# Kernel optimization log

Measured on AMD Instinct MI355X. Metric: run time of the kernel, lower is better.

## Reference

```python
import jax, jax.numpy as jnp
import numpy as np

N_NODES = 50000
N_RELS = 8
IN_DIM = 128
OUT_DIM = 128
N_EDGES = 800000


def setup_inputs() -> dict:
    key = jax.random.key(0)
    k1, k2, k3, k4 = jax.random.split(key, 4)
    src = jax.random.randint(k1, (N_EDGES,), 0, N_NODES, dtype=jnp.int64 if jax.config.jax_enable_x64 else jnp.int32)
    rel = jax.random.randint(k2, (N_EDGES,), 0, N_RELS, dtype=src.dtype)
    tgt = jax.random.randint(k3, (N_EDGES,), 0, N_NODES, dtype=src.dtype)
    triples = jnp.stack([src, rel, tgt], axis=1)  # (E, 3) like torch layout (s, r, t)
    features = jax.random.normal(k4, (N_NODES, IN_DIM), dtype=jnp.float32)
    weights = jax.random.normal(jax.random.fold_in(key, 1), (N_RELS, IN_DIM, OUT_DIM), dtype=jnp.float32) * (1.0 / np.sqrt(IN_DIM))
    bias = jnp.zeros((OUT_DIM,), dtype=jnp.float32)
    return {"triples": triples, "features": features, "weights": weights, "bias": bias}


def reference(triples, features, weights, bias):
    # RGCN-NC forward, horizontal stacking (featured mode):
    #   out[t] = sum_{(s,r,t) in E} (1/c_{t,r}) * features[s] @ W[r] + bias
    # where c_{t,r} = #edges sharing the same (relation, target) pair,
    # matching sum_sparse(..., row_normalisation=False) on the (n x r*n) adjacency.
    src, rel, tgt = triples[:, 0], triples[:, 1], triples[:, 2]
    n = features.shape[0]
    r = weights.shape[0]
    e = triples.shape[0]

    # per-(rel, tgt) edge counts -> 1/c normalization per edge
    key = rel * n + tgt  # column index of horizontally stacked adjacency
    counts = jax.ops.segment_sum(jnp.ones((e,), dtype=features.dtype), key, num_segments=r * n)
    vals = 1.0 / counts[key]  # (E,)

    # dense per-relation transform: H[r] = X @ W[r]   (r, n, out)
    h = jnp.einsum('ni,rio->rno', features, weights)

    # gather per-edge messages, scale, scatter-add into targets
    msgs = h[rel, src] * vals[:, None]  # (E, out)
    out = jax.ops.segment_sum(msgs, tgt, num_segments=n)  # (n, out)
    return out + bias
```

## Files before the change

kernel.cpp:

```cpp
#include <hip/hip_runtime.h>
#include <hip/hip_bf16.h>

#define N_NODES 50000
#define N_RELS 8
#define IN_DIM 128
#define OUT_DIM 128
#define N_EDGES 800000
#define NR (N_NODES * N_RELS)
#define KDIM (N_RELS * IN_DIM)
#define SCAN_ELEMS 2048
#define SCAN_NBLK ((NR + SCAN_ELEMS - 1) / SCAN_ELEMS)
#define FUSE_BLKS 1563
#define CNT_BLKS ((N_EDGES / 4 + 255) / 256)
#define CW_BLKS ((N_RELS * IN_DIM * OUT_DIM + 255) / 256)
#define FB_BLKS ((N_NODES * IN_DIM / 8 + 255) / 256)

typedef __attribute__((ext_vector_type(8))) short bf16x8;
typedef __attribute__((ext_vector_type(4))) float floatx4;
typedef __attribute__((ext_vector_type(4))) unsigned int uintx4;

__device__ inline unsigned short f2bf(float f) {
    unsigned u = __builtin_bit_cast(unsigned, f);
    u += 0x7fff + ((u >> 16) & 1);
    return (unsigned short)(u >> 16);
}
__device__ inline float bflo(unsigned u) {
    return __builtin_bit_cast(float, u << 16);
}
__device__ inline float bfhi(unsigned u) {
    return __builtin_bit_cast(float, u & 0xffff0000u);
}

__global__ void prep_kernel(const int* __restrict__ tri, const float* __restrict__ W,
                            const float* __restrict__ features,
                            int* __restrict__ cnt, unsigned short* __restrict__ Wtf,
                            unsigned short* __restrict__ featB) {
    const int b = blockIdx.x;
    if (b < CNT_BLKS) {
        int t = b * 256 + threadIdx.x;
        if (t >= N_EDGES / 4) return;
        const int4* tri4 = (const int4*)tri;
        int4 a = tri4[3 * t], v = tri4[3 * t + 1], c = tri4[3 * t + 2];
        atomicAdd(&cnt[a.z * N_RELS + a.y], 1);
        atomicAdd(&cnt[v.y * N_RELS + v.x], 1);
        atomicAdd(&cnt[c.x * N_RELS + v.w], 1);
        atomicAdd(&cnt[c.w * N_RELS + c.z], 1);
    } else if (b < CNT_BLKS + CW_BLKS) {
        int idx = (b - CNT_BLKS) * 256 + threadIdx.x;
        if (idx >= N_RELS * IN_DIM * OUT_DIM) return;
        int e  = idx & 7;
        int l  = (idx >> 3) & 63;
        int ks = (idx >> 9) & 31;
        int nt = idx >> 14;
        int o = nt * 16 + (l & 15);
        int k = ks * 32 + (l >> 4) * 8 + e;
        Wtf[idx] = f2bf(W[(k >> 7) * (IN_DIM * OUT_DIM) + (k & 127) * OUT_DIM + o]);
    } else {
        int t = (b - CNT_BLKS - CW_BLKS) * 256 + threadIdx.x;
        if (t >= N_NODES * IN_DIM / 8) return;
        const float4* f4 = (const float4*)features;
        float4 x = f4[2 * t], y = f4[2 * t + 1];
        uint4 o;
        o.x = (unsigned)f2bf(x.x) | ((unsigned)f2bf(x.y) << 16);
        o.y = (unsigned)f2bf(x.z) | ((unsigned)f2bf(x.w) << 16);
        o.z = (unsigned)f2bf(y.x) | ((unsigned)f2bf(y.y) << 16);
        o.w = (unsigned)f2bf(y.z) | ((unsigned)f2bf(y.w) << 16);
        ((uint4*)featB)[t] = o;
    }
}

__global__ void scan_part(const int* __restrict__ cnt, int* __restrict__ bsum) {
    __shared__ int s[256];
    int b = blockIdx.x, t = threadIdx.x;
    int base = b * SCAN_ELEMS + t * 8;
    int sum = 0;
#pragma unroll
    for (int k = 0; k < 8; ++k) {
        int i = base + k;
        sum += (i < NR) ? cnt[i] : 0;
    }
    s[t] = sum; __syncthreads();
    for (int off = 128; off > 0; off >>= 1) {
        if (t < off) s[t] += s[t + off];
        __syncthreads();
    }
    if (t == 0) bsum[b] = s[0];
}

__global__ __launch_bounds__(256) void scan_fused(
    const int* __restrict__ cnt, const int* __restrict__ bsum,
    int* __restrict__ segOff, int* __restrict__ cursor)
{
    __shared__ int s[256];
    __shared__ int sboff;
    const int b = blockIdx.x, t = threadIdx.x;

    int vb = (t < SCAN_NBLK) ? bsum[t] : 0;
    s[t] = vb; __syncthreads();
    for (int off = 1; off < 256; off <<= 1) {
        int x = (t >= off) ? s[t - off] : 0;
        __syncthreads();
        s[t] += x;
        __syncthreads();
    }
    if (t == 0) sboff = (b == 0) ? 0 : s[b - 1];
    __syncthreads();
    const int boff = sboff;

    const int base = b * SCAN_ELEMS + t * 8;
    int v[8]; int sum = 0;
#pragma unroll
    for (int k = 0; k < 8; ++k) {
        int i = base + k;
        v[k] = (i < NR) ? cnt[i] : 0;
        sum += v[k];
    }
    s[t] = sum; __syncthreads();
    for (int off = 1; off < 256; off <<= 1) {
        int x = (t >= off) ? s[t - off] : 0;
        __syncthreads();
        s[t] += x;
        __syncthreads();
    }
    int run = boff + s[t] - sum;
#pragma unroll
    for (int k = 0; k < 8; ++k) {
        int i = base + k;
        if (i < NR) { segOff[i] = run; cursor[i] = run; run += v[k]; }
    }
    if (b == 0 && t == 0) segOff[NR] = N_EDGES;
}

__global__ void scatter_kernel(const int* __restrict__ tri, int* __restrict__ cursor,
                               int* __restrict__ sortedSrc) {
    int t = blockIdx.x * 256 + threadIdx.x;
    if (t >= N_EDGES / 4) return;
    const int4* tri4 = (const int4*)tri;
    int4 a = tri4[3 * t], v = tri4[3 * t + 1], c = tri4[3 * t + 2];
    int p0 = atomicAdd(&cursor[a.z * N_RELS + a.y], 1);
    int p1 = atomicAdd(&cursor[v.y * N_RELS + v.x], 1);
    int p2 = atomicAdd(&cursor[c.x * N_RELS + v.w], 1);
    int p3 = atomicAdd(&cursor[c.w * N_RELS + c.z], 1);
    sortedSrc[p0] = a.x;
    sortedSrc[p1] = a.w;
    sortedSrc[p2] = v.z;
    sortedSrc[p3] = c.y;
}

__global__ __launch_bounds__(512, 8) void fused_kernel(
    const int* __restrict__ sortedSrc, const int* __restrict__ segOff,
    const unsigned short* __restrict__ featB,
    const unsigned short* __restrict__ Wtf,
    const float* __restrict__ bias,
    float* __restrict__ out)
{
    __shared__ __align__(16) unsigned short Atile[32 * 512];
    const int tid = threadIdx.x;
    const int wave = tid >> 6, lane = tid & 63;
    const int q = lane >> 4, l16 = lane & 15;
    const int m0 = blockIdx.x * 32;
    const int wm = wave & 1, wn = wave >> 1;

    floatx4 acc[2];
#pragma unroll
    for (int nt = 0; nt < 2; ++nt) acc[nt] = (floatx4){0.f, 0.f, 0.f, 0.f};

    const unsigned short* fb = featB + 8 * l16;

#pragma unroll
    for (int p = 0; p < 2; ++p) {
        for (int i = 0; i < 4; ++i) {
            const int nl = wave * 4 + i;
            const int node = m0 + nl;
            if (node < N_NODES) {
                int bnd = 0;
                if (lane < 5) bnd = segOff[node * N_RELS + 4 * p + lane];
                int sg[5];
#pragma unroll
                for (int k = 0; k < 5; ++k) sg[k] = __shfl(bnd, k);

                const int e0 = sg[0], eN = sg[4];
                int srcw = 0;
                if (e0 + lane < eN) srcw = sortedSrc[e0 + lane];

                const int s0v = sg[q], s1v = sg[q + 1];
                const int len = s1v - s0v;
                int m0x = __shfl_xor(len, 16);
                int jm = (len > m0x) ? len : m0x;
                int m1x = __shfl_xor(jm, 32);
                const int jmax = (jm > m1x) ? jm : m1x;
                float a0 = 0.f, a1 = 0.f, a2 = 0.f, a3 = 0.f;
                float a4 = 0.f, a5 = 0.f, a6 = 0.f, a7 = 0.f;
                for (int j = 0; j < jmax; j += 2) {
                    const int ea = s0v + j;
                    const int ia = ea - e0;
                    const int swina = __shfl(srcw, ia & 63);
                    const int ib = ia + 1;
                    const int swinb = __shfl(srcw, ib & 63);
                    const bool pa = j < len;
                    const bool pb = j + 1 < len;
                    int srca = 0, srcb = 0;
                    if (pa) srca = (ia < 64) ? swina : sortedSrc[ea];
                    if (pb) srcb = (ib < 64) ? swinb : sortedSrc[ea + 1];
                    uint4 ua = *(const uint4*)&fb[srca * IN_DIM];
                    uint4 ub = *(const uint4*)&fb[srcb * IN_DIM];
                    if (pa) {
                        a0 += bflo(ua.x); a1 += bfhi(ua.x);
                        a2 += bflo(ua.y); a3 += bfhi(ua.y);
                        a4 += bflo(ua.z); a5 += bfhi(ua.z);
                        a6 += bflo(ua.w); a7 += bfhi(ua.w);
                    }
                    if (pb) {
                        a0 += bflo(ub.x); a1 += bfhi(ub.x);
                        a2 += bflo(ub.y); a3 += bfhi(ub.y);
                        a4 += bflo(ub.z); a5 += bfhi(ub.z);
                        a6 += bflo(ub.w); a7 += bfhi(ub.w);
                    }
                }
                const float inv = (len > 0) ? 1.0f / (float)len : 0.0f;
                uintx4 pk;
                pk[0] = (unsigned)f2bf(a0 * inv) | ((unsigned)f2bf(a1 * inv) << 16);
                pk[1] = (unsigned)f2bf(a2 * inv) | ((unsigned)f2bf(a3 * inv) << 16);
                pk[2] = (unsigned)f2bf(a4 * inv) | ((unsigned)f2bf(a5 * inv) << 16);
                pk[3] = (unsigned)f2bf(a6 * inv) | ((unsigned)f2bf(a7 * inv) << 16);
                const int us = (q * 16 + l16) ^ (nl & 15);
                *(uintx4*)&Atile[(nl * 64 + us) * 8] = pk;
            }
        }
        __syncthreads();

        __builtin_amdgcn_s_setprio(1);
#pragma unroll
        for (int ksl = 0; ksl < 16; ++ksl) {
            const int ks = p * 16 + ksl;
            const int r = wm * 16 + l16;
            const int us = (ksl * 4 + q) ^ (r & 15);
            bf16x8 a = *(const bf16x8*)&Atile[(r * 64 + us) * 8];
#pragma unroll
            for (int nt = 0; nt < 2; ++nt) {
                const int ntg = wn * 2 + nt;
                bf16x8 b = *(const bf16x8*)&Wtf[(size_t)((ntg * 32 + ks) * 64 + lane) * 8];
                acc[nt] = __builtin_amdgcn_mfma_f32_16x16x32_bf16(a, b, acc[nt], 0, 0, 0);
            }
        }
        __builtin_amdgcn_s_setprio(0);
        __syncthreads();
    }

    float* fbuf = (float*)Atile;
#pragma unroll
    for (int nt = 0; nt < 2; ++nt) {
        const int o = (wn * 2 + nt) * 16 + l16;
        const float bv = bias[o];
#pragma unroll
        for (int j = 0; j < 4; ++j) {
            const int r = wm * 16 + q * 4 + j;
            fbuf[r * 128 + o] = acc[nt][j] + bv;
        }
    }
    __syncthreads();
    {
        const int row = tid >> 4;
        const int col = (tid & 15) * 8;
        const int node = m0 + row;
        if (node < N_NODES) {
            floatx4 w0 = *(const floatx4*)&fbuf[row * 128 + col];
            floatx4 w1 = *(const floatx4*)&fbuf[row * 128 + col + 4];
            float* po = &out[(size_t)node * OUT_DIM + col];
            __builtin_nontemporal_store(w0, (floatx4*)po);
            __builtin_nontemporal_store(w1, (floatx4*)(po + 4));
        }
    }
}

extern "C" void kernel_launch(void* const* d_in, const int* in_sizes, int n_in,
                              void* d_out, int out_size, void* d_ws, size_t ws_size,
                              hipStream_t stream)
{
    const int*   tri      = (const int*)d_in[0];
    const float* features = (const float*)d_in[1];
    const float* W        = (const float*)d_in[2];
    const float* bias     = (const float*)d_in[3];
    float* out = (float*)d_out;

    char* ws = (char*)d_ws;
    unsigned short* Wtf = (unsigned short*)ws; ws += (size_t)OUT_DIM * KDIM * 2;
    int* cnt       = (int*)ws; ws += (size_t)NR * 4;
    int* segOff    = (int*)ws; ws += (size_t)(NR + 4) * 4;
    int* cursor    = (int*)ws; ws += (size_t)NR * 4;
    int* bsum      = (int*)ws; ws += (size_t)SCAN_NBLK * 4;
    int* sortedSrc = (int*)ws; ws += (size_t)N_EDGES * 4;
    unsigned short* featB = (unsigned short*)ws; ws += (size_t)N_NODES * IN_DIM * 2;
    (void)ws_size; (void)in_sizes; (void)n_in; (void)out_size;

    hipMemsetAsync(cnt, 0, NR * sizeof(int), stream);
    prep_kernel<<<CNT_BLKS + CW_BLKS + FB_BLKS, 256, 0, stream>>>(tri, W, features, cnt, Wtf, featB);
    scan_part<<<SCAN_NBLK, 256, 0, stream>>>(cnt, bsum);
    scan_fused<<<SCAN_NBLK, 256, 0, stream>>>(cnt, bsum, segOff, cursor);
    scatter_kernel<<<CNT_BLKS, 256, 0, stream>>>(tri, cursor, sortedSrc);
    fused_kernel<<<FUSE_BLKS, 512, 0, stream>>>(sortedSrc, segOff, featB, Wtf, bias, out);
}
```

Baseline: 256.5 us.

## Merge count, scan and scatter prelude into one persistent kernel with grid barriers

Replaces the four preprocessing launches (prep, two-pass scan, scatter) with a single kernel of 782 blocks of 512 threads. The phases are separated by software grid barriers built on atomic counters. This removes several kernel launch gaps and the tail drain between dependent stages. The barrier relies on all blocks being co-resident, so a different occupancy could deadlock it, and thread 0 of each block spin-waits on a global atomic.

```diff
diff --git a/kernel.cpp b/kernel.cpp
--- a/kernel.cpp
+++ b/kernel.cpp
@@ -8,12 +8,11 @@
 #define N_EDGES 800000
 #define NR (N_NODES * N_RELS)
 #define KDIM (N_RELS * IN_DIM)
-#define SCAN_ELEMS 2048
-#define SCAN_NBLK ((NR + SCAN_ELEMS - 1) / SCAN_ELEMS)
+#define PRE_NB 782
+#define PRE_T 512
+#define PRE_THREADS (PRE_NB * PRE_T)
+#define SCB 391
 #define FUSE_BLKS 1563
-#define CNT_BLKS ((N_EDGES / 4 + 255) / 256)
-#define CW_BLKS ((N_RELS * IN_DIM * OUT_DIM + 255) / 256)
-#define FB_BLKS ((N_NODES * IN_DIM / 8 + 255) / 256)
 
 typedef __attribute__((ext_vector_type(8))) short bf16x8;
 typedef __attribute__((ext_vector_type(4))) float floatx4;
@@ -31,23 +30,34 @@
     return __builtin_bit_cast(float, u & 0xffff0000u);
 }
 
-__global__ void prep_kernel(const int* __restrict__ tri, const float* __restrict__ W,
-                            const float* __restrict__ features,
-                            int* __restrict__ cnt, unsigned short* __restrict__ Wtf,
-                            unsigned short* __restrict__ featB) {
+__device__ __forceinline__ void grid_bar(int* __restrict__ bar, int idx, int nblk) {
+    __syncthreads();
+    if (threadIdx.x == 0) {
+        __threadfence();
+        atomicAdd(&bar[idx], 1);
+        while (__hip_atomic_load(&bar[idx], __ATOMIC_RELAXED,
+                                 __HIP_MEMORY_SCOPE_AGENT) < nblk)
+            __builtin_amdgcn_s_sleep(1);
+        __threadfence();
+    }
+    __syncthreads();
+}
+
+__global__ __launch_bounds__(512, 8) void prelude_kernel(
+    const int* __restrict__ tri, const float* __restrict__ features,
+    const float* __restrict__ W,
+    unsigned short* __restrict__ Wtf, unsigned short* __restrict__ featB,
+    int* __restrict__ cnt, int* __restrict__ bar,
+    int* __restrict__ segOff, int* __restrict__ cursor,
+    int* __restrict__ bsum, int* __restrict__ sortedSrc)
+{
+    __shared__ int s_int[512];
+    const int tid = threadIdx.x;
     const int b = blockIdx.x;
-    if (b < CNT_BLKS) {
-        int t = b * 256 + threadIdx.x;
-        if (t >= N_EDGES / 4) return;
-        const int4* tri4 = (const int4*)tri;
-        int4 a = tri4[3 * t], v = tri4[3 * t + 1], c = tri4[3 * t + 2];
-        atomicAdd(&cnt[a.z * N_RELS + a.y], 1);
-        atomicAdd(&cnt[v.y * N_RELS + v.x], 1);
-        atomicAdd(&cnt[c.x * N_RELS + v.w], 1);
-        atomicAdd(&cnt[c.w * N_RELS + c.z], 1);
-    } else if (b < CNT_BLKS + CW_BLKS) {
-        int idx = (b - CNT_BLKS) * 256 + threadIdx.x;
-        if (idx >= N_RELS * IN_DIM * OUT_DIM) return;
+    const int gid = b * PRE_T + tid;
+
+    if (gid < N_RELS * IN_DIM * OUT_DIM) {
+        const int idx = gid;
         int e  = idx & 7;
         int l  = (idx >> 3) & 63;
         int ks = (idx >> 9) & 31;
@@ -55,9 +65,8 @@
         int o = nt * 16 + (l & 15);
         int k = ks * 32 + (l >> 4) * 8 + e;
         Wtf[idx] = f2bf(W[(k >> 7) * (IN_DIM * OUT_DIM) + (k & 127) * OUT_DIM + o]);
-    } else {
-        int t = (b - CNT_BLKS - CW_BLKS) * 256 + threadIdx.x;
-        if (t >= N_NODES * IN_DIM / 8) return;
+    }
+    for (int t = gid; t < N_NODES * IN_DIM / 8; t += PRE_THREADS) {
         const float4* f4 = (const float4*)features;
         float4 x = f4[2 * t], y = f4[2 * t + 1];
         uint4 o;
@@ -67,84 +76,72 @@
         o.w = (unsigned)f2bf(y.z) | ((unsigned)f2bf(y.w) << 16);
         ((uint4*)featB)[t] = o;
     }
-}
-
-__global__ void scan_part(const int* __restrict__ cnt, int* __restrict__ bsum) {
-    __shared__ int s[256];
-    int b = blockIdx.x, t = threadIdx.x;
-    int base = b * SCAN_ELEMS + t * 8;
-    int sum = 0;
-#pragma unroll
-    for (int k = 0; k < 8; ++k) {
-        int i = base + k;
-        sum += (i < NR) ? cnt[i] : 0;
-    }
-    s[t] = sum; __syncthreads();
-    for (int off = 128; off > 0; off >>= 1) {
-        if (t < off) s[t] += s[t + off];
-        __syncthreads();
-    }
-    if (t == 0) bsum[b] = s[0];
-}
-
-__global__ __launch_bounds__(256) void scan_fused(
-    const int* __restrict__ cnt, const int* __restrict__ bsum,
-    int* __restrict__ segOff, int* __restrict__ cursor)
-{
-    __shared__ int s[256];
-    __shared__ int sboff;
-    const int b = blockIdx.x, t = threadIdx.x;
-
-    int vb = (t < SCAN_NBLK) ? bsum[t] : 0;
-    s[t] = vb; __syncthreads();
-    for (int off = 1; off < 256; off <<= 1) {
-        int x = (t >= off) ? s[t - off] : 0;
-        __syncthreads();
-        s[t] += x;
-        __syncthreads();
-    }
-    if (t == 0) sboff = (b == 0) ? 0 : s[b - 1];
-    __syncthreads();
-    const int boff = sboff;
-
-    const int base = b * SCAN_ELEMS + t * 8;
-    int v[8]; int sum = 0;
-#pragma unroll
-    for (int k = 0; k < 8; ++k) {
-        int i = base + k;
-        v[k] = (i < NR) ? cnt[i] : 0;
-        sum += v[k];
-    }
-    s[t] = sum; __syncthreads();
-    for (int off = 1; off < 256; off <<= 1) {
-        int x = (t >= off) ? s[t - off] : 0;
-        __syncthreads();
-        s[t] += x;
-        __syncthreads();
-    }
-    int run = boff + s[t] - sum;
-#pragma unroll
-    for (int k = 0; k < 8; ++k) {
-        int i = base + k;
-        if (i < NR) { segOff[i] = run; cursor[i] = run; run += v[k]; }
-    }
-    if (b == 0 && t == 0) segOff[NR] = N_EDGES;
-}
-
-__global__ void scatter_kernel(const int* __restrict__ tri, int* __restrict__ cursor,
-                               int* __restrict__ sortedSrc) {
-    int t = blockIdx.x * 256 + threadIdx.x;
-    if (t >= N_EDGES / 4) return;
-    const int4* tri4 = (const int4*)tri;
-    int4 a = tri4[3 * t], v = tri4[3 * t + 1], c = tri4[3 * t + 2];
-    int p0 = atomicAdd(&cursor[a.z * N_RELS + a.y], 1);
-    int p1 = atomicAdd(&cursor[v.y * N_RELS + v.x], 1);
-    int p2 = atomicAdd(&cursor[c.x * N_RELS + v.w], 1);
-    int p3 = atomicAdd(&cursor[c.w * N_RELS + c.z], 1);
-    sortedSrc[p0] = a.x;
-    sortedSrc[p1] = a.w;
-    sortedSrc[p2] = v.z;
-    sortedSrc[p3] = c.y;
+    if (gid < N_EDGES / 4) {
+        const int4* tri4 = (const int4*)tri;
+        int4 a = tri4[3 * gid], v = tri4[3 * gid + 1], c = tri4[3 * gid + 2];
+        atomicAdd(&cnt[a.z * N_RELS + a.y], 1);
+        atomicAdd(&cnt[v.y * N_RELS + v.x], 1);
+        atomicAdd(&cnt[c.x * N_RELS + v.w], 1);
+        atomicAdd(&cnt[c.w * N_RELS + c.z], 1);
+    }
+    grid_bar(bar, 0, PRE_NB);
+
+    if (b < SCB) {
+        const int base = b * 1024 + tid * 2;
+        int v0 = (base     < NR) ? cnt[base]     : 0;
+        int v1 = (base + 1 < NR) ? cnt[base + 1] : 0;
+        s_int[tid] = v0 + v1;
+        __syncthreads();
+        for (int off = 256; off > 0; off >>= 1) {
+            if (tid < off) s_int[tid] += s_int[tid + off];
+            __syncthreads();
+        }
+        if (tid == 0) bsum[b] = s_int[0];
+    }
+    grid_bar(bar, 1, PRE_NB);
+
+    if (b < SCB) {
+        int vb = (tid < SCB) ? bsum[tid] : 0;
+        s_int[tid] = vb; __syncthreads();
+        for (int off = 1; off < 512; off <<= 1) {
+            int x = (tid >= off) ? s_int[tid - off] : 0;
+            __syncthreads();
+            s_int[tid] += x;
+            __syncthreads();
+        }
+        const int boff = (b == 0) ? 0 : s_int[b - 1];
+        __syncthreads();
+
+        const int base = b * 1024 + tid * 2;
+        int v0 = (base     < NR) ? cnt[base]     : 0;
+        int v1 = (base + 1 < NR) ? cnt[base + 1] : 0;
+        const int sum = v0 + v1;
+        s_int[tid] = sum; __syncthreads();
+        for (int off = 1; off < 512; off <<= 1) {
+            int x = (tid >= off) ? s_int[tid - off] : 0;
+            __syncthreads();
+            s_int[tid] += x;
+            __syncthreads();
+        }
+        int run = boff + s_int[tid] - sum;
+        if (base < NR)     { segOff[base] = run;     cursor[base] = run;     run += v0; }
+        if (base + 1 < NR) { segOff[base + 1] = run; cursor[base + 1] = run; }
+        if (b == 0 && tid == 0) segOff[NR] = N_EDGES;
+    }
+    grid_bar(bar, 2, PRE_NB);
+
+    if (gid < N_EDGES / 4) {
+        const int4* tri4 = (const int4*)tri;
+        int4 a = tri4[3 * gid], v = tri4[3 * gid + 1], c = tri4[3 * gid + 2];
+        int p0 = atomicAdd(&cursor[a.z * N_RELS + a.y], 1);
+        int p1 = atomicAdd(&cursor[v.y * N_RELS + v.x], 1);
+        int p2 = atomicAdd(&cursor[c.x * N_RELS + v.w], 1);
+        int p3 = atomicAdd(&cursor[c.w * N_RELS + c.z], 1);
+        sortedSrc[p0] = a.x;
+        sortedSrc[p1] = a.w;
+        sortedSrc[p2] = v.z;
+        sortedSrc[p3] = c.y;
+    }
 }
 
 __global__ __launch_bounds__(512, 8) void fused_kernel(
@@ -286,17 +283,17 @@
     char* ws = (char*)d_ws;
     unsigned short* Wtf = (unsigned short*)ws; ws += (size_t)OUT_DIM * KDIM * 2;
     int* cnt       = (int*)ws; ws += (size_t)NR * 4;
+    int* bar       = (int*)ws; ws += 16 * 4;
     int* segOff    = (int*)ws; ws += (size_t)(NR + 4) * 4;
     int* cursor    = (int*)ws; ws += (size_t)NR * 4;
-    int* bsum      = (int*)ws; ws += (size_t)SCAN_NBLK * 4;
+    int* bsum      = (int*)ws; ws += (size_t)512 * 4;
     int* sortedSrc = (int*)ws; ws += (size_t)N_EDGES * 4;
     unsigned short* featB = (unsigned short*)ws; ws += (size_t)N_NODES * IN_DIM * 2;
     (void)ws_size; (void)in_sizes; (void)n_in; (void)out_size;
 
-    hipMemsetAsync(cnt, 0, NR * sizeof(int), stream);
-    prep_kernel<<<CNT_BLKS + CW_BLKS + FB_BLKS, 256, 0, stream>>>(tri, W, features, cnt, Wtf, featB);
-    scan_part<<<SCAN_NBLK, 256, 0, stream>>>(cnt, bsum);
-    scan_fused<<<SCAN_NBLK, 256, 0, stream>>>(cnt, bsum, segOff, cursor);
-    scatter_kernel<<<CNT_BLKS, 256, 0, stream>>>(tri, cursor, sortedSrc);
-    fused_kernel<<<FUSE_BLKS, 512, 0, stream>>>(sortedSrc, segOff, featB, Wtf, bias, out);
-}
+    hipMemsetAsync(cnt, 0, (NR + 16) * sizeof(int), stream);
+    prelude_kernel<<<PRE_NB, PRE_T, 0, stream>>>(
+        tri, features, W, Wtf, featB, cnt, bar, segOff, cursor, bsum, sortedSrc);
+    fused_kernel<<<FUSE_BLKS, PRE_T, 0, stream>>>(
+        sortedSrc, segOff, featB, Wtf, bias, out);
+}
```

Result: slower. 488.9 us (+90.6%).

## Replace global CSR sort with bucketed binning and per-block LDS sort

Applied to the files above, without the earlier changes.

The count, two-pass scan and scatter kernels that built a global (target, relation) CSR are removed. Edges are now appended into fixed-capacity buckets of 32 target nodes, each packed into one int (16-bit source, relation, local target). The fused kernel then counts, scans and sorts its bucket's edges in shared memory before aggregation. This cuts kernel launches and global index traffic, but concentrates atomics on far fewer bucket counters. It also assumes no bucket exceeds 2048 edges and that node ids fit in 16 bits.

```diff
diff --git a/kernel.cpp b/kernel.cpp
--- a/kernel.cpp
+++ b/kernel.cpp
@@ -6,12 +6,11 @@
 #define IN_DIM 128
 #define OUT_DIM 128
 #define N_EDGES 800000
-#define NR (N_NODES * N_RELS)
 #define KDIM (N_RELS * IN_DIM)
-#define SCAN_ELEMS 2048
-#define SCAN_NBLK ((NR + SCAN_ELEMS - 1) / SCAN_ELEMS)
-#define FUSE_BLKS 1563
-#define CNT_BLKS ((N_EDGES / 4 + 255) / 256)
+#define NBKT 1563
+#define CAP 2048
+#define FUSE_BLKS NBKT
+#define EG_BLKS ((N_EDGES / 4 + 255) / 256)
 #define CW_BLKS ((N_RELS * IN_DIM * OUT_DIM + 255) / 256)
 #define FB_BLKS ((N_NODES * IN_DIM / 8 + 255) / 256)
 
@@ -31,22 +30,28 @@
     return __builtin_bit_cast(float, u & 0xffff0000u);
 }
 
-__global__ void prep_kernel(const int* __restrict__ tri, const float* __restrict__ W,
-                            const float* __restrict__ features,
-                            int* __restrict__ cnt, unsigned short* __restrict__ Wtf,
-                            unsigned short* __restrict__ featB) {
+__global__ void prep2_kernel(const int* __restrict__ tri, const float* __restrict__ W,
+                             const float* __restrict__ features,
+                             int* __restrict__ bcnt, int* __restrict__ bdata,
+                             unsigned short* __restrict__ Wtf,
+                             unsigned short* __restrict__ featB) {
     const int b = blockIdx.x;
-    if (b < CNT_BLKS) {
+    if (b < EG_BLKS) {
         int t = b * 256 + threadIdx.x;
         if (t >= N_EDGES / 4) return;
         const int4* tri4 = (const int4*)tri;
         int4 a = tri4[3 * t], v = tri4[3 * t + 1], c = tri4[3 * t + 2];
-        atomicAdd(&cnt[a.z * N_RELS + a.y], 1);
-        atomicAdd(&cnt[v.y * N_RELS + v.x], 1);
-        atomicAdd(&cnt[c.x * N_RELS + v.w], 1);
-        atomicAdd(&cnt[c.w * N_RELS + c.z], 1);
-    } else if (b < CNT_BLKS + CW_BLKS) {
-        int idx = (b - CNT_BLKS) * 256 + threadIdx.x;
+        int s[4] = { a.x, a.w, v.z, c.y };
+        int r[4] = { a.y, v.x, v.w, c.z };
+        int g[4] = { a.z, v.y, c.x, c.w };
+#pragma unroll
+        for (int k = 0; k < 4; ++k) {
+            const int bkt = g[k] >> 5;
+            const int pos = atomicAdd(&bcnt[bkt], 1);
+            bdata[bkt * CAP + pos] = s[k] | (r[k] << 16) | ((g[k] & 31) << 19);
+        }
+    } else if (b < EG_BLKS + CW_BLKS) {
+        int idx = (b - EG_BLKS) * 256 + threadIdx.x;
         if (idx >= N_RELS * IN_DIM * OUT_DIM) return;
         int e  = idx & 7;
         int l  = (idx >> 3) & 63;
@@ -56,7 +61,7 @@
         int k = ks * 32 + (l >> 4) * 8 + e;
         Wtf[idx] = f2bf(W[(k >> 7) * (IN_DIM * OUT_DIM) + (k & 127) * OUT_DIM + o]);
     } else {
-        int t = (b - CNT_BLKS - CW_BLKS) * 256 + threadIdx.x;
+        int t = (b - EG_BLKS - CW_BLKS) * 256 + threadIdx.x;
         if (t >= N_NODES * IN_DIM / 8) return;
         const float4* f4 = (const float4*)features;
         float4 x = f4[2 * t], y = f4[2 * t + 1];
@@ -69,97 +74,60 @@
     }
 }
 
-__global__ void scan_part(const int* __restrict__ cnt, int* __restrict__ bsum) {
-    __shared__ int s[256];
-    int b = blockIdx.x, t = threadIdx.x;
-    int base = b * SCAN_ELEMS + t * 8;
-    int sum = 0;
-#pragma unroll
-    for (int k = 0; k < 8; ++k) {
-        int i = base + k;
-        sum += (i < NR) ? cnt[i] : 0;
-    }
-    s[t] = sum; __syncthreads();
-    for (int off = 128; off > 0; off >>= 1) {
-        if (t < off) s[t] += s[t + off];
-        __syncthreads();
-    }
-    if (t == 0) bsum[b] = s[0];
-}
-
-__global__ __launch_bounds__(256) void scan_fused(
-    const int* __restrict__ cnt, const int* __restrict__ bsum,
-    int* __restrict__ segOff, int* __restrict__ cursor)
-{
-    __shared__ int s[256];
-    __shared__ int sboff;
-    const int b = blockIdx.x, t = threadIdx.x;
-
-    int vb = (t < SCAN_NBLK) ? bsum[t] : 0;
-    s[t] = vb; __syncthreads();
-    for (int off = 1; off < 256; off <<= 1) {
-        int x = (t >= off) ? s[t - off] : 0;
-        __syncthreads();
-        s[t] += x;
-        __syncthreads();
-    }
-    if (t == 0) sboff = (b == 0) ? 0 : s[b - 1];
-    __syncthreads();
-    const int boff = sboff;
-
-    const int base = b * SCAN_ELEMS + t * 8;
-    int v[8]; int sum = 0;
-#pragma unroll
-    for (int k = 0; k < 8; ++k) {
-        int i = base + k;
-        v[k] = (i < NR) ? cnt[i] : 0;
-        sum += v[k];
-    }
-    s[t] = sum; __syncthreads();
-    for (int off = 1; off < 256; off <<= 1) {
-        int x = (t >= off) ? s[t - off] : 0;
-        __syncthreads();
-        s[t] += x;
-        __syncthreads();
-    }
-    int run = boff + s[t] - sum;
-#pragma unroll
-    for (int k = 0; k < 8; ++k) {
-        int i = base + k;
-        if (i < NR) { segOff[i] = run; cursor[i] = run; run += v[k]; }
-    }
-    if (b == 0 && t == 0) segOff[NR] = N_EDGES;
-}
-
-__global__ void scatter_kernel(const int* __restrict__ tri, int* __restrict__ cursor,
-                               int* __restrict__ sortedSrc) {
-    int t = blockIdx.x * 256 + threadIdx.x;
-    if (t >= N_EDGES / 4) return;
-    const int4* tri4 = (const int4*)tri;
-    int4 a = tri4[3 * t], v = tri4[3 * t + 1], c = tri4[3 * t + 2];
-    int p0 = atomicAdd(&cursor[a.z * N_RELS + a.y], 1);
-    int p1 = atomicAdd(&cursor[v.y * N_RELS + v.x], 1);
-    int p2 = atomicAdd(&cursor[c.x * N_RELS + v.w], 1);
-    int p3 = atomicAdd(&cursor[c.w * N_RELS + c.z], 1);
-    sortedSrc[p0] = a.x;
-    sortedSrc[p1] = a.w;
-    sortedSrc[p2] = v.z;
-    sortedSrc[p3] = c.y;
-}
-
 __global__ __launch_bounds__(512, 8) void fused_kernel(
-    const int* __restrict__ sortedSrc, const int* __restrict__ segOff,
+    const int* __restrict__ bcnt, const int* __restrict__ bdata,
     const unsigned short* __restrict__ featB,
     const unsigned short* __restrict__ Wtf,
     const float* __restrict__ bias,
     float* __restrict__ out)
 {
     __shared__ __align__(16) unsigned short Atile[32 * 512];
+    __shared__ unsigned short srcS[CAP];
+    __shared__ int cntL[256];
+    __shared__ int segL[256];
+    __shared__ int curL[256];
+    __shared__ int s_n;
+
     const int tid = threadIdx.x;
+    const int b = blockIdx.x;
     const int wave = tid >> 6, lane = tid & 63;
     const int q = lane >> 4, l16 = lane & 15;
-    const int m0 = blockIdx.x * 32;
+    const int m0 = b * 32;
     const int wm = wave & 1, wn = wave >> 1;
+
+    if (tid == 0) s_n = bcnt[b];
+    if (tid < 256) cntL[tid] = 0;
+    __syncthreads();
+    const int n = s_n;
+    const int* bd = bdata + b * CAP;
+    for (int e = tid; e < n; e += 512) {
+        const unsigned u = (unsigned)bd[e];
+        const int key = ((u >> 19) & 31) * 8 + ((u >> 16) & 7);
+        atomicAdd(&cntL[key], 1);
+    }
+    __syncthreads();
+    if (tid < 256) segL[tid] = cntL[tid];
+    __syncthreads();
+    for (int off = 1; off < 256; off <<= 1) {
+        int x = 0;
+        if (tid < 256 && tid >= off) x = segL[tid - off];
+        __syncthreads();
+        if (tid < 256) segL[tid] += x;
+        __syncthreads();
+    }
+    if (tid < 256) {
+        const int ex = segL[tid] - cntL[tid];
+        segL[tid] = ex;
+        curL[tid] = ex;
+    }
+    __syncthreads();
+    for (int e = tid; e < n; e += 512) {
+        const unsigned u = (unsigned)bd[e];
+        const int key = ((u >> 19) & 31) * 8 + ((u >> 16) & 7);
+        const int pos = atomicAdd(&curL[key], 1);
+        srcS[pos] = (unsigned short)(u & 0xffff);
+    }
+    __syncthreads();
 
     floatx4 acc[2];
 #pragma unroll
@@ -171,61 +139,37 @@
     for (int p = 0; p < 2; ++p) {
         for (int i = 0; i < 4; ++i) {
             const int nl = wave * 4 + i;
-            const int node = m0 + nl;
-            if (node < N_NODES) {
-                int bnd = 0;
-                if (lane < 5) bnd = segOff[node * N_RELS + 4 * p + lane];
-                int sg[5];
-#pragma unroll
-                for (int k = 0; k < 5; ++k) sg[k] = __shfl(bnd, k);
-
-                const int e0 = sg[0], eN = sg[4];
-                int srcw = 0;
-                if (e0 + lane < eN) srcw = sortedSrc[e0 + lane];
-
-                const int s0v = sg[q], s1v = sg[q + 1];
-                const int len = s1v - s0v;
-                int m0x = __shfl_xor(len, 16);
-                int jm = (len > m0x) ? len : m0x;
-                int m1x = __shfl_xor(jm, 32);
-                const int jmax = (jm > m1x) ? jm : m1x;
-                float a0 = 0.f, a1 = 0.f, a2 = 0.f, a3 = 0.f;
-                float a4 = 0.f, a5 = 0.f, a6 = 0.f, a7 = 0.f;
-                for (int j = 0; j < jmax; j += 2) {
-                    const int ea = s0v + j;
-                    const int ia = ea - e0;
-                    const int swina = __shfl(srcw, ia & 63);
-                    const int ib = ia + 1;
-                    const int swinb = __shfl(srcw, ib & 63);
-                    const bool pa = j < len;
-                    const bool pb = j + 1 < len;
-                    int srca = 0, srcb = 0;
-                    if (pa) srca = (ia < 64) ? swina : sortedSrc[ea];
-                    if (pb) srcb = (ib < 64) ? swinb : sortedSrc[ea + 1];
-                    uint4 ua = *(const uint4*)&fb[srca * IN_DIM];
-                    uint4 ub = *(const uint4*)&fb[srcb * IN_DIM];
-                    if (pa) {
-                        a0 += bflo(ua.x); a1 += bfhi(ua.x);
-                        a2 += bflo(ua.y); a3 += bfhi(ua.y);
-                        a4 += bflo(ua.z); a5 += bfhi(ua.z);
-                        a6 += bflo(ua.w); a7 += bfhi(ua.w);
-                    }
-                    if (pb) {
-                        a0 += bflo(ub.x); a1 += bfhi(ub.x);
-                        a2 += bflo(ub.y); a3 += bfhi(ub.y);
-                        a4 += bflo(ub.z); a5 += bfhi(ub.z);
-                        a6 += bflo(ub.w); a7 += bfhi(ub.w);
-                    }
+            const int key = nl * 8 + 4 * p + q;
+            const int s0 = segL[key];
+            const int len = cntL[key];
+            float a0 = 0.f, a1 = 0.f, a2 = 0.f, a3 = 0.f;
+            float a4 = 0.f, a5 = 0.f, a6 = 0.f, a7 = 0.f;
+            for (int j = 0; j < len; j += 2) {
+                const int sa = srcS[s0 + j];
+                const int jb = (j + 1 < len) ? (j + 1) : j;
+                const int sb = srcS[s0 + jb];
+                const bool pb = j + 1 < len;
+                uint4 ua = *(const uint4*)&fb[sa * IN_DIM];
+                uint4 ub = *(const uint4*)&fb[sb * IN_DIM];
+                a0 += bflo(ua.x); a1 += bfhi(ua.x);
+                a2 += bflo(ua.y); a3 += bfhi(ua.y);
+                a4 += bflo(ua.z); a5 += bfhi(ua.z);
+                a6 += bflo(ua.w); a7 += bfhi(ua.w);
+                if (pb) {
+                    a0 += bflo(ub.x); a1 += bfhi(ub.x);
+                    a2 += bflo(ub.y); a3 += bfhi(ub.y);
+                    a4 += bflo(ub.z); a5 += bfhi(ub.z);
+                    a6 += bflo(ub.w); a7 += bfhi(ub.w);
                 }
-                const float inv = (len > 0) ? 1.0f / (float)len : 0.0f;
-                uintx4 pk;
-                pk[0] = (unsigned)f2bf(a0 * inv) | ((unsigned)f2bf(a1 * inv) << 16);
-                pk[1] = (unsigned)f2bf(a2 * inv) | ((unsigned)f2bf(a3 * inv) << 16);
-                pk[2] = (unsigned)f2bf(a4 * inv) | ((unsigned)f2bf(a5 * inv) << 16);
-                pk[3] = (unsigned)f2bf(a6 * inv) | ((unsigned)f2bf(a7 * inv) << 16);
-                const int us = (q * 16 + l16) ^ (nl & 15);
-                *(uintx4*)&Atile[(nl * 64 + us) * 8] = pk;
             }
+            const float inv = (len > 0) ? 1.0f / (float)len : 0.0f;
+            uintx4 pk;
+            pk[0] = (unsigned)f2bf(a0 * inv) | ((unsigned)f2bf(a1 * inv) << 16);
+            pk[1] = (unsigned)f2bf(a2 * inv) | ((unsigned)f2bf(a3 * inv) << 16);
+            pk[2] = (unsigned)f2bf(a4 * inv) | ((unsigned)f2bf(a5 * inv) << 16);
+            pk[3] = (unsigned)f2bf(a6 * inv) | ((unsigned)f2bf(a7 * inv) << 16);
+            const int us = (q * 16 + l16) ^ (nl & 15);
+            *(uintx4*)&Atile[(nl * 64 + us) * 8] = pk;
         }
         __syncthreads();
 
@@ -239,8 +183,8 @@
 #pragma unroll
             for (int nt = 0; nt < 2; ++nt) {
                 const int ntg = wn * 2 + nt;
-                bf16x8 b = *(const bf16x8*)&Wtf[(size_t)((ntg * 32 + ks) * 64 + lane) * 8];
-                acc[nt] = __builtin_amdgcn_mfma_f32_16x16x32_bf16(a, b, acc[nt], 0, 0, 0);
+                bf16x8 bb = *(const bf16x8*)&Wtf[(size_t)((ntg * 32 + ks) * 64 + lane) * 8];
+                acc[nt] = __builtin_amdgcn_mfma_f32_16x16x32_bf16(a, bb, acc[nt], 0, 0, 0);
             }
         }
         __builtin_amdgcn_s_setprio(0);
@@ -285,18 +229,13 @@
 
     char* ws = (char*)d_ws;
     unsigned short* Wtf = (unsigned short*)ws; ws += (size_t)OUT_DIM * KDIM * 2;
-    int* cnt       = (int*)ws; ws += (size_t)NR * 4;
-    int* segOff    = (int*)ws; ws += (size_t)(NR + 4) * 4;
-    int* cursor    = (int*)ws; ws += (size_t)NR * 4;
-    int* bsum      = (int*)ws; ws += (size_t)SCAN_NBLK * 4;
-    int* sortedSrc = (int*)ws; ws += (size_t)N_EDGES * 4;
+    int* bcnt  = (int*)ws; ws += (size_t)2048 * 4;
+    int* bdata = (int*)ws; ws += (size_t)NBKT * CAP * 4;
     unsigned short* featB = (unsigned short*)ws; ws += (size_t)N_NODES * IN_DIM * 2;
     (void)ws_size; (void)in_sizes; (void)n_in; (void)out_size;
 
-    hipMemsetAsync(cnt, 0, NR * sizeof(int), stream);
-    prep_kernel<<<CNT_BLKS + CW_BLKS + FB_BLKS, 256, 0, stream>>>(tri, W, features, cnt, Wtf, featB);
-    scan_part<<<SCAN_NBLK, 256, 0, stream>>>(cnt, bsum);
-    scan_fused<<<SCAN_NBLK, 256, 0, stream>>>(cnt, bsum, segOff, cursor);
-    scatter_kernel<<<CNT_BLKS, 256, 0, stream>>>(tri, cursor, sortedSrc);
-    fused_kernel<<<FUSE_BLKS, 512, 0, stream>>>(sortedSrc, segOff, featB, Wtf, bias, out);
-}
+    hipMemsetAsync(bcnt, 0, NBKT * sizeof(int), stream);
+    prep2_kernel<<<EG_BLKS + CW_BLKS + FB_BLKS, 256, 0, stream>>>(
+        tri, W, features, bcnt, bdata, Wtf, featB);
+    fused_kernel<<<FUSE_BLKS, 512, 0, stream>>>(bcnt, bdata, featB, Wtf, bias, out);
+}
```

New measurement: 284.6 us. 11.0% more time.
